# Kernel optimization log

Hardware: AMD Instinct MI355X
Metric: run time of the kernel (lower is better)

Reference implementation:

```python
import jax, jax.numpy as jnp
import numpy as np
from jax import lax

D = 256      # key/query dim
D_F = 256    # diff feature channels
C_TOK = 1    # leading context tokens in query_vit
EPS = 1e-6


def conv2d(x, w, b, pad):
    out = lax.conv_general_dilated(x, w, (1, 1), [(pad, pad), (pad, pad)],
                                   dimension_numbers=('NCHW', 'OIHW', 'NCHW'))
    return out + b[None, :, None, None]


def gn1(x, g, b):
    # GroupNorm with 1 group: normalize over (C,H,W) per sample
    mu = jnp.mean(x, axis=(1, 2, 3), keepdims=True)
    var = jnp.var(x, axis=(1, 2, 3), keepdims=True)
    xn = (x - mu) * lax.rsqrt(var + EPS)
    return xn * g[None, :, None, None] + b[None, :, None, None]


def resize_bilinear_ac(x, Ho, Wo):
    # F.interpolate(mode='bilinear', align_corners=True)
    B, C, H, W = x.shape
    ys = jnp.linspace(0.0, H - 1.0, Ho)
    xs = jnp.linspace(0.0, W - 1.0, Wo)
    y0 = jnp.floor(ys).astype(jnp.int32)
    y1 = jnp.minimum(y0 + 1, H - 1)
    wy = (ys - y0)[None, None, :, None]
    x0 = jnp.floor(xs).astype(jnp.int32)
    x1 = jnp.minimum(x0 + 1, W - 1)
    wx = (xs - x0)[None, None, None, :]
    r = x[:, :, y0, :] * (1.0 - wy) + x[:, :, y1, :] * wy
    return r[:, :, :, x0] * (1.0 - wx) + r[:, :, :, x1] * wx


def setup_inputs() -> dict:
    key = jax.random.key(0)
    ks = jax.random.split(key, 12)
    B, Hd, Wd, Ht, Wt = 8, 64, 64, 32, 32

    def kaiming(k, shape, fan_in):
        return jax.random.normal(k, shape, jnp.float32) * np.sqrt(2.0 / fan_in)

    return {
        'query_vit': jax.random.normal(ks[0], (B, C_TOK + Ht * Wt, D), jnp.float32),
        'feat_diff_cat': jax.random.normal(ks[1], (B, 5 * D_F, Hd, Wd), jnp.float32),
        'rb_w1': kaiming(ks[2], (D_F, 5 * D_F, 3, 3), 5 * D_F * 9), 'rb_b1': jnp.zeros((D_F,), jnp.float32),
        'rb_w2': kaiming(ks[3], (D_F, D_F, 3, 3), D_F * 9), 'rb_b2': jnp.zeros((D_F,), jnp.float32),
        'rb_ws': kaiming(ks[4], (D_F, 5 * D_F, 1, 1), 5 * D_F), 'rb_bs': jnp.zeros((D_F,), jnp.float32),
        'ln_g': jnp.ones((D_F,), jnp.float32), 'ln_b': jnp.zeros((D_F,), jnp.float32),
        'key_w': kaiming(ks[5], (D, D_F, 1, 1), D_F), 'key_b': jnp.zeros((D,), jnp.float32),
        'val_w': kaiming(ks[6], (D_F, D_F, 1, 1), D_F), 'val_b': jnp.zeros((D_F,), jnp.float32),
        'dh0_w': kaiming(ks[7], (D_F, D_F, 3, 3), D_F * 9), 'dh0_b': jnp.zeros((D_F,), jnp.float32),
        'dh1_w': kaiming(ks[8], (D_F, D_F, 3, 3), D_F * 9), 'dh1_b': jnp.zeros((D_F,), jnp.float32),
    }


def reference(query_vit, feat_diff_cat, rb_w1, rb_b1, rb_w2, rb_b2, rb_ws, rb_bs,
              ln_g, ln_b, key_w, key_b, val_w, val_b, dh0_w, dh0_b, dh1_w, dh1_b):
    B, _, h_diff, w_diff = feat_diff_cat.shape
    N = query_vit.shape[1] - C_TOK
    h_trm = w_trm = int(N ** 0.5)

    # ResBlock_ysh(D_f*5 -> D_f): conv3x3 + relu + conv3x3, 1x1-projected residual
    h = jax.nn.relu(conv2d(feat_diff_cat, rb_w1, rb_b1, 1))
    h = conv2d(h, rb_w2, rb_b2, 1)
    feat_diff = jax.nn.relu(h + conv2d(feat_diff_cat, rb_ws, rb_bs, 0))

    fln = gn1(feat_diff, ln_g, ln_b)
    key_diff = conv2d(fln, key_w, key_b, 0).reshape(B, D, -1)          # (B, D, HW)
    value_diff = conv2d(fln, val_w, val_b, 0).reshape(B, D_F, -1)      # (B, Df, HW)
    value_diff = jnp.transpose(value_diff, (0, 2, 1))                  # (B, HW, Df)

    # cross attention: (B, C+N, D) @ (B, D, HW) -> softmax -> @ (B, HW, Df)
    scores = jnp.einsum('bnd,bdm->bnm', query_vit, key_diff) * (D ** -0.5)
    attn = jax.nn.softmax(scores, axis=-1)
    out_cross = jnp.einsum('bnm,bmf->bnf', attn, value_diff)           # (B, C+N, Df)

    out_cross_c = out_cross[:, :C_TOK, :]
    out_p = jnp.transpose(out_cross[:, C_TOK:, :], (0, 2, 1)).reshape(B, D_F, h_trm, w_trm)
    out_p = jax.nn.relu(conv2d(out_p, dh0_w, dh0_b, 1))
    out_p = resize_bilinear_ac(out_p, h_diff, w_diff)
    out_p = out_p + feat_diff                                          # DropPath(0) = identity
    out_p = jax.nn.relu(conv2d(gn1(out_p, ln_g, ln_b), dh1_w, dh1_b, 1)) + out_p
    return out_cross_c, out_p
```

## Files before the change

### kernel.cpp

```cpp
#include <hip/hip_runtime.h>
#include <cstdint>
#include <cstddef>

typedef __attribute__((ext_vector_type(4))) float     f32x4;
typedef __attribute__((ext_vector_type(8))) __bf16    bf16x8;
typedef __attribute__((ext_vector_type(8))) short     short8;
typedef __attribute__((ext_vector_type(4))) unsigned short u16x4;
typedef unsigned short u16;

__device__ __forceinline__ float b2f(u16 u) {
  unsigned x = ((unsigned)u) << 16;
  float f;
  __builtin_memcpy(&f, &x, 4);
  return f;
}
__device__ __forceinline__ u16 f2b(float f) {
  unsigned u;
  __builtin_memcpy(&u, &f, 4);
  return (u16)((u + 0x7FFFu + ((u >> 16) & 1u)) >> 16);
}

struct GP {
  const u16*  A;
  const u16*  B;
  const float* bias;
  const void* aux;
  void*       C;
  float*      out0;
  float*      st;
  long long   aBS, bBS, cBS, auxBS, biasBS;
  int Ktot, Mrows, ldc;
  int cin, logW, wpad, poff;
  float scale;
};

#define GLDS16(g, l)                                                        \
  __builtin_amdgcn_global_load_lds(                                         \
      (const void __attribute__((address_space(1)))*)(g),                   \
      (void __attribute__((address_space(3)))*)(l), 16, 0, 0)

struct G256 {
  const u16* A;
  const u16* B;
  float* P;
  long long aBS;
  int Ktot, cin, logW, wpad, poff;
};

__global__ __launch_bounds__(512, 2) void k_gemm256(G256 gp) {
  const int tid = threadIdx.x;
  const int l = tid & 63, w = tid >> 6;
  const int lr = l & 15, lc = l >> 4;
  const int id = blockIdx.x;
  const int xcd = id & 7, slot = id >> 3;
  const int sp = xcd >> 2;
  const int u = (xcd & 3) * 32 + slot;
  const int mt = u & 15;
  const int b = u >> 4;
  const int m0 = mt << 8;
  const int wm = w >> 2, wn = w & 3;

  __shared__ __align__(16) u16 sm[2][32768];
  u16* smb = &sm[0][0];

  f32x4 acc[8][4];
#pragma unroll
  for (int i = 0; i < 8; ++i)
#pragma unroll
    for (int j = 0; j < 4; ++j) acc[i][j] = (f32x4){0.f, 0.f, 0.f, 0.f};

  const u16* Ab = gp.A + (size_t)b * gp.aBS;
  const int slotl = l & 3;
  const u16* aS[2];
  const u16* bS[2];
#pragma unroll
  for (int j = 0; j < 2; ++j) {
    const int r = j * 128 + w * 16 + (l >> 2);
    const int p = m0 + r;
    const int y = p >> gp.logW, x = p & ((1 << gp.logW) - 1);
    const int sw = (slotl ^ ((r >> 1) & 3)) << 3;
    aS[j] = Ab + (size_t)((y + gp.poff) * gp.wpad + (x + gp.poff)) * gp.cin + sw;
    bS[j] = gp.B + (size_t)r * gp.Ktot + sw;
  }
  auto dstA = [&](int buf, int ks, int j) -> u16* {
    return smb + buf * 32768 + ks * 8192 + (j * 128 + w * 16) * 32 + l * 8;
  };
  auto dstB = [&](int buf, int ks, int j) -> u16* {
    return smb + buf * 32768 + 16384 + ks * 8192 + (j * 128 + w * 16) * 32 + l * 8;
  };

  const int Thalf = (gp.Ktot >> 6) >> 1;
  const int kt0 = sp * Thalf;
  int off = kt0 << 6;
  int tap = off / gp.cin;
  int kcS = off - tap * gp.cin;
  int dxS = tap % 3;
  int tapS = (tap / 3) * gp.wpad + dxS;
  int ktS = kt0;

  auto adv = [&](int& kA, int& kB) {
    kB = ktS << 6;
    kA = tapS * gp.cin + kcS;
    kcS += 64;
    if (kcS == gp.cin) {
      kcS = 0; ++dxS; ++tapS;
      if (dxS == 3) { dxS = 0; tapS += gp.wpad - 3; }
    }
    ++ktS;
  };

  {
    int kA, kB;
    adv(kA, kB);
    GLDS16(aS[0] + kA, dstA(0, 0, 0));
    GLDS16(aS[1] + kA, dstA(0, 0, 1));
    GLDS16(bS[0] + kB, dstB(0, 0, 0));
    GLDS16(bS[1] + kB, dstB(0, 0, 1));
    GLDS16(aS[0] + kA + 32, dstA(0, 1, 0));
    GLDS16(aS[1] + kA + 32, dstA(0, 1, 1));
    GLDS16(bS[0] + kB + 32, dstB(0, 1, 0));
    GLDS16(bS[1] + kB + 32, dstB(0, 1, 1));
  }
  asm volatile("s_waitcnt vmcnt(0)" ::: "memory");
  __builtin_amdgcn_s_barrier();

  const int NT = Thalf;
  for (int t = 0; t < NT; ++t) {
    const int buf = t & 1;
    const char* base = (const char*)smb + buf * 65536;
    const bool pf = (t + 1 < NT);
    if (pf) {
      int kA, kB;
      adv(kA, kB);
      GLDS16(aS[0] + kA, dstA(buf ^ 1, 0, 0));
      GLDS16(aS[1] + kA, dstA(buf ^ 1, 0, 1));
      GLDS16(bS[0] + kB, dstB(buf ^ 1, 0, 0));
      GLDS16(bS[1] + kB, dstB(buf ^ 1, 0, 1));
      GLDS16(aS[0] + kA + 32, dstA(buf ^ 1, 1, 0));
      GLDS16(aS[1] + kA + 32, dstA(buf ^ 1, 1, 1));
      GLDS16(bS[0] + kB + 32, dstB(buf ^ 1, 1, 0));
      GLDS16(bS[1] + kB + 32, dstB(buf ^ 1, 1, 1));
    }
    bf16x8 bv0[4], bv1[4];
#pragma unroll
    for (int ni = 0; ni < 4; ++ni) {
      const int row = wn * 64 + ni * 16 + lr;
      const int sw = (lc ^ ((row >> 1) & 3)) << 4;
      bv0[ni] = *(const bf16x8*)(base + 32768 + row * 64 + sw);
      bv1[ni] = *(const bf16x8*)(base + 49152 + row * 64 + sw);
    }
#pragma unroll
    for (int mq = 0; mq < 2; ++mq) {
      bf16x8 a0[4], a1[4];
#pragma unroll
      for (int mi = 0; mi < 4; ++mi) {
        const int row = wm * 128 + (mq * 4 + mi) * 16 + lr;
        const int sw = (lc ^ ((row >> 1) & 3)) << 4;
        a0[mi] = *(const bf16x8*)(base + row * 64 + sw);
        a1[mi] = *(const bf16x8*)(base + 16384 + row * 64 + sw);
      }
#pragma unroll
      for (int mi = 0; mi < 4; ++mi)
#pragma unroll
        for (int ni = 0; ni < 4; ++ni)
          acc[mq * 4 + mi][ni] = __builtin_amdgcn_mfma_f32_16x16x32_bf16(
              a0[mi], bv0[ni], acc[mq * 4 + mi][ni], 0, 0, 0);
#pragma unroll
      for (int mi = 0; mi < 4; ++mi)
#pragma unroll
        for (int ni = 0; ni < 4; ++ni)
          acc[mq * 4 + mi][ni] = __builtin_amdgcn_mfma_f32_16x16x32_bf16(
              a1[mi], bv1[ni], acc[mq * 4 + mi][ni], 0, 0, 0);
    }
    asm volatile("s_waitcnt vmcnt(0)" ::: "memory");
    __builtin_amdgcn_s_barrier();
  }

  float* P = gp.P + ((size_t)sp * 128 + b * 16 + mt) * 65536;
#pragma unroll
  for (int mi = 0; mi < 8; ++mi)
#pragma unroll
    for (int ni = 0; ni < 4; ++ni) {
      const int ncol = wn * 64 + ni * 16 + lr;
      const int mloc = wm * 128 + mi * 16 + lc * 4;
#pragma unroll
      for (int r = 0; r < 4; ++r)
        P[(size_t)(mloc + r) * 256 + ncol] = acc[mi][ni][r];
    }
}

__global__ __launch_bounds__(256) void k_reduceH1(const float* __restrict__ P,
                                                  const float* __restrict__ bias,
                                                  u16* __restrict__ o) {
  const int i4 = blockIdx.x * 256 + threadIdx.x;
  const int flat = i4 << 2;
  const int n0 = flat & 255;
  const int mloc = (flat >> 8) & 255;
  const int gm = flat >> 16;
  const f32x4 a = *(const f32x4*)(P + (size_t)gm * 65536 + mloc * 256 + n0);
  const f32x4 c = *(const f32x4*)(P + (size_t)(128 + gm) * 65536 + mloc * 256 + n0);
  const f32x4 bb = *(const f32x4*)(bias + n0);
  const int batch = gm >> 4;
  const int mg = (gm & 15) * 256 + mloc;
  const int y = mg >> 6, x = mg & 63;
  u16x4 r;
#pragma unroll
  for (int k = 0; k < 4; ++k) r[k] = f2b(fmaxf(a[k] + c[k] + bb[k], 0.f));
  *(u16x4*)(o + ((size_t)batch * 4356 + (size_t)(y + 1) * 66 + x + 1) * 256 + n0) = r;
}

template <int AMODE, int CW>
__global__ __launch_bounds__(512, 2) void k_gemm8(GP gp) {
  const int tid = threadIdx.x;
  const int l = tid & 63, w = tid >> 6;
  const int b = blockIdx.z;
  const int m0 = blockIdx.x * 128;
  const int wm = w >> 2, wn = w & 3;
  const int lr = l & 15, lc = l >> 4;

  __shared__ __align__(16) u16 sm[2][24576];

  f32x4 acc[4][4];
#pragma unroll
  for (int i = 0; i < 4; ++i)
#pragma unroll
    for (int j = 0; j < 4; ++j) acc[i][j] = (f32x4){0.f, 0.f, 0.f, 0.f};

  const u16* Ab = gp.A + (size_t)b * gp.aBS;
  const u16* Bb = gp.B + (size_t)b * gp.bBS;
  const int scoff = (((tid & 7) ^ ((tid >> 3) & 7)) << 3);

  const u16* aP[2];
  const u16* aP2[2];
#pragma unroll
  for (int i = 0; i < 2; ++i) {
    const int p = m0 + i * 64 + (tid >> 3);
    const int y = p >> 6, x = p & 63;
    aP[i] = Ab + (size_t)(y * 66 + x) * gp.cin + scoff;
    if (AMODE == 2) {
      const u16* Xb = (const u16*)gp.aux + (size_t)b * gp.auxBS;
      aP2[i] = Xb + (size_t)((y + 1) * 66 + (x + 1)) * 1280 + scoff;
    }
  }
  const u16* bP[4];
#pragma unroll
  for (int i = 0; i < 4; ++i)
    bP[i] = Bb + (size_t)(i * 64 + (tid >> 3)) * gp.Ktot + scoff;

  const int NT = gp.Ktot >> 6;
  const int seg1t = (AMODE == 2) ? 36 : 0x7fffffff;
  int kcS = 0, tapS = 0, dxS = 0, nstg = 0;

  auto stage = [&](int buf) {
    const int kt = nstg++;
    const int kB = kt << 6;
    u16* sA = &sm[buf][0] + (w << 9);
    u16* sB = &sm[buf][8192] + (w << 9);
    if (AMODE == 2 && kt >= seg1t) {
      const int kA = (kt - seg1t) << 6;
      GLDS16(aP2[0] + kA, sA);
      GLDS16(aP2[1] + kA, sA + 4096);
    } else {
      const int kA = tapS * gp.cin + kcS;
      kcS += 64;
      if (kcS == gp.cin) {
        kcS = 0; ++dxS; ++tapS;
        if (dxS == 3) { dxS = 0; tapS += 63; }
      }
      GLDS16(aP[0] + kA, sA);
      GLDS16(aP[1] + kA, sA + 4096);
    }
    GLDS16(bP[0] + kB, sB);
    GLDS16(bP[1] + kB, sB + 4096);
    GLDS16(bP[2] + kB, sB + 8192);
    GLDS16(bP[3] + kB, sB + 12288);
  };

  stage(0);
  asm volatile("s_waitcnt vmcnt(0)" ::: "memory");
  __builtin_amdgcn_s_barrier();

  for (int t = 0; t < NT; ++t) {
    const int buf = t & 1;
    const u16* sAc = &sm[buf][0];
    const u16* sBc = &sm[buf][8192];
    if (t + 1 < NT) stage(buf ^ 1);

    bf16x8 av0[4], av1[4], bv0[4], bv1[4];
#pragma unroll
    for (int mi = 0; mi < 4; ++mi) {
      const int row = wm * 64 + mi * 16 + lr;
      av0[mi] = *(const bf16x8*)(sAc + row * 64 + (((0 + lc) ^ (row & 7)) << 3));
      av1[mi] = *(const bf16x8*)(sAc + row * 64 + (((4 + lc) ^ (row & 7)) << 3));
    }
#pragma unroll
    for (int ni = 0; ni < 4; ++ni) {
      const int row = wn * 64 + ni * 16 + lr;
      bv0[ni] = *(const bf16x8*)(sBc + row * 64 + (((0 + lc) ^ (row & 7)) << 3));
      bv1[ni] = *(const bf16x8*)(sBc + row * 64 + (((4 + lc) ^ (row & 7)) << 3));
    }
#pragma unroll
    for (int mi = 0; mi < 4; ++mi)
#pragma unroll
      for (int ni = 0; ni < 4; ++ni)
        acc[mi][ni] = __builtin_amdgcn_mfma_f32_16x16x32_bf16(
            av0[mi], bv0[ni], acc[mi][ni], 0, 0, 0);
#pragma unroll
    for (int mi = 0; mi < 4; ++mi)
#pragma unroll
      for (int ni = 0; ni < 4; ++ni)
        acc[mi][ni] = __builtin_amdgcn_mfma_f32_16x16x32_bf16(
            av1[mi], bv1[ni], acc[mi][ni], 0, 0, 0);
    asm volatile("s_waitcnt vmcnt(0)" ::: "memory");
    __builtin_amdgcn_s_barrier();
  }

  float lsum = 0.f, lsq = 0.f;
#pragma unroll
  for (int mi = 0; mi < 4; ++mi) {
#pragma unroll
    for (int ni = 0; ni < 4; ++ni) {
      const int ncol = wn * 64 + ni * 16 + lr;
      const int mbase = m0 + wm * 64 + mi * 16 + lc * 4;
      const float bv_ = gp.bias[ncol];
      if constexpr (CW == 8) {
        float* F = (float*)gp.C + (size_t)b * gp.cBS;
        u16* FB = (u16*)gp.out0 + (size_t)b * gp.cBS;
#pragma unroll
        for (int r = 0; r < 4; ++r) {
          float v = fmaxf(acc[mi][ni][r] + bv_, 0.f);
          const size_t idx = (size_t)(mbase + r) * 256 + ncol;
          F[idx] = v;
          FB[idx] = f2b(v);
          lsum += v;
          lsq += v * v;
        }
      } else {
        float* Cf =
            (float*)gp.C + (size_t)b * gp.cBS + (size_t)ncol * 4096 + mbase;
        const float* mid = (const float*)gp.aux + (size_t)b * gp.auxBS;
        f32x4 o;
#pragma unroll
        for (int r = 0; r < 4; ++r) {
          float v = fmaxf(acc[mi][ni][r] + bv_, 0.f);
          o[r] = v + mid[(size_t)(mbase + r) * 256 + ncol];
        }
        *(f32x4*)Cf = o;
      }
    }
  }
  if constexpr (CW == 8) {
    __syncthreads();
#pragma unroll
    for (int o = 32; o; o >>= 1) {
      lsum += __shfl_down(lsum, o);
      lsq += __shfl_down(lsq, o);
    }
    float* red = (float*)&sm[0][0];
    if (l == 0) { red[w * 2] = lsum; red[w * 2 + 1] = lsq; }
    __syncthreads();
    if (tid == 0) {
      float s = 0.f, s2 = 0.f;
#pragma unroll
      for (int k = 0; k < 8; ++k) { s += red[k * 2]; s2 += red[k * 2 + 1]; }
      atomicAdd(&gp.st[b * 2], s);
      atomicAdd(&gp.st[b * 2 + 1], s2);
    }
  }
}

template <int AMODE, int CW, bool RELU>
__global__ __launch_bounds__(256, 2) void k_gemm(GP gp) {
  const int tid = threadIdx.x;
  const int l = tid & 63, w = tid >> 6;
  const int b = blockIdx.z;
  const int m0 = blockIdx.x * 128, n0 = blockIdx.y * 128;
  const int wm = w >> 1, wn = w & 1;

  __shared__ __align__(16) u16 smA[128 * 64];
  __shared__ __align__(16) u16 smB[128 * 64];

  f32x4 acc[4][4];
#pragma unroll
  for (int i = 0; i < 4; ++i)
#pragma unroll
    for (int j = 0; j < 4; ++j) acc[i][j] = (f32x4){0.f, 0.f, 0.f, 0.f};

  const u16* Ab = gp.A + (size_t)b * gp.aBS;
  const u16* Bb = gp.B + (size_t)b * gp.bBS;

  const int scoff = (((l & 7) ^ (l >> 3)) << 3);

  const u16* aRow[4];
  const u16* bRow[4];
  u16* ldsA[4];
  u16* ldsB[4];
#pragma unroll
  for (int i = 0; i < 4; ++i) {
    const int r = w * 32 + i * 8 + (l >> 3);
    bRow[i] = Bb + (size_t)(n0 + r) * gp.Ktot + scoff;
    const int p = m0 + r;
    if (AMODE == 0) {
      const int pc = p < gp.Mrows ? p : gp.Mrows - 1;
      aRow[i] = Ab + (size_t)pc * gp.Ktot + scoff;
    } else {
      const int y = p >> gp.logW, x = p & ((1 << gp.logW) - 1);
      const int icoord = (y + gp.poff) * gp.wpad + (x + gp.poff);
      aRow[i] = Ab + (size_t)icoord * gp.cin + scoff;
    }
    ldsA[i] = smA + (w * 32 + i * 8) * 64;
    ldsB[i] = smB + (w * 32 + i * 8) * 64;
  }

  const int ktiles = gp.Ktot >> 6;
  int tap_off = 0, dx = 0, kc = 0;

  for (int kt = 0; kt < ktiles; ++kt) {
    int koffA;
    if (AMODE == 0)
      koffA = kt << 6;
    else
      koffA = tap_off * gp.cin + kc;
    const int koffB = kt << 6;
#pragma unroll
    for (int i = 0; i < 4; ++i) GLDS16(aRow[i] + koffA, ldsA[i]);
#pragma unroll
    for (int i = 0; i < 4; ++i) GLDS16(bRow[i] + koffB, ldsB[i]);

    if (AMODE == 1) {
      kc += 64;
      if (kc == gp.cin) {
        kc = 0;
        ++dx;
        ++tap_off;
        if (dx == 3) { dx = 0; tap_off += gp.wpad - 3; }
      }
    }

    __syncthreads();
#pragma unroll
    for (int ks = 0; ks < 2; ++ks) {
      bf16x8 av[4], bv[4];
      const int cc = (ks << 2) + (l >> 4);
#pragma unroll
      for (int mi = 0; mi < 4; ++mi) {
        const int row = wm * 64 + mi * 16 + (l & 15);
        av[mi] = *(const bf16x8*)((const char*)smA + (row << 7) +
                                  ((cc ^ (row & 7)) << 4));
      }
#pragma unroll
      for (int ni = 0; ni < 4; ++ni) {
        const int row = wn * 64 + ni * 16 + (l & 15);
        bv[ni] = *(const bf16x8*)((const char*)smB + (row << 7) +
                                  ((cc ^ (row & 7)) << 4));
      }
#pragma unroll
      for (int mi = 0; mi < 4; ++mi)
#pragma unroll
        for (int ni = 0; ni < 4; ++ni)
          acc[mi][ni] = __builtin_amdgcn_mfma_f32_16x16x32_bf16(
              av[mi], bv[ni], acc[mi][ni], 0, 0, 0);
    }
    __syncthreads();
  }

#pragma unroll
  for (int mi = 0; mi < 4; ++mi) {
#pragma unroll
    for (int ni = 0; ni < 4; ++ni) {
      const int ncol = n0 + wn * 64 + ni * 16 + (l & 15);
      const int mbase = m0 + wm * 64 + mi * 16 + ((l >> 4) << 2);
      const float bv_ =
          gp.bias ? gp.bias[(size_t)b * gp.biasBS + ncol] : 0.f;

      if constexpr (CW == 7) {
        u16* base = (u16*)gp.C;
        if (ncol < 256) {
#pragma unroll
          for (int r = 0; r < 4; ++r)
            base[(size_t)b * 1048576 + (size_t)(mbase + r) * 256 + ncol] =
                f2b(acc[mi][ni][r] + bv_);
        } else {
          u16x4 pk;
#pragma unroll
          for (int r = 0; r < 4; ++r) pk[r] = f2b(acc[mi][ni][r] + bv_);
          *(u16x4*)(base + 8388608 + (size_t)b * 1048576 +
                    (size_t)(ncol - 256) * 4096 + mbase) = pk;
        }
      } else {
#pragma unroll
        for (int reg = 0; reg < 4; ++reg) {
          const int mrow = mbase + reg;
          if (mrow >= gp.Mrows) continue;
          float v = acc[mi][ni][reg] * gp.scale + bv_;
          if (RELU) v = v > 0.f ? v : 0.f;
          if constexpr (CW == 0) {
            ((u16*)gp.C)[(size_t)b * gp.cBS + (size_t)mrow * gp.ldc + ncol] =
                f2b(v);
          } else if constexpr (CW == 4) {
            if (mrow == 0) {
              gp.out0[(size_t)b * 256 + ncol] = v;
            } else {
              const int p = mrow - 1, y = p >> 5, x = p & 31;
              ((u16*)gp.C)[(size_t)b * gp.cBS +
                           (size_t)((y + 1) * 34 + (x + 1)) * 256 + ncol] =
                  f2b(v);
            }
          } else if constexpr (CW == 5) {
            ((float*)gp.C)[(size_t)b * gp.cBS + (size_t)mrow * 256 + ncol] = v;
          }
        }
      }
    }
  }
}


__global__ __launch_bounds__(256) void k_prep_x(const float* __restrict__ x,
                                                u16* __restrict__ o) {
  __shared__ float t[32][65];
  const int b = blockIdx.z, c0 = blockIdx.y << 5, y = blockIdx.x;
  const float* src = x + ((size_t)b * 1280 + c0) * 4096 + (size_t)y * 64;
#pragma unroll
  for (int i = 0; i < 8; ++i) {
    const int idx = threadIdx.x + (i << 8);
    const int c = idx >> 6, xx = idx & 63;
    t[c][xx] = src[(size_t)c * 4096 + xx];
  }
  __syncthreads();
  u16* dst = o + ((size_t)b * 4356 + (size_t)(y + 1) * 66 + 1) * 1280 + c0;
  const int xx = threadIdx.x >> 2;
  const int cq = (threadIdx.x & 3) << 3;
  short8 pk;
#pragma unroll
  for (int j = 0; j < 8; ++j) pk[j] = (short)f2b(t[cq + j][xx]);
  *(short8*)(dst + (size_t)xx * 1280 + cq) = pk;
}

__device__ __forceinline__ void zb1(u16* p, int P, int C, int idx) {
  const int per_img = (4 * P - 4) * C;
  const int b = idx / per_img;
  const int r = idx % per_img;
  const int pix = r / C, c = r % C;
  int y, x;
  const int Pm = P - 1;
  if (pix < P) { y = 0; x = pix; }
  else if (pix < 2 * P) { y = Pm; x = pix - P; }
  else if (pix < 3 * P - 2) { y = pix - 2 * P + 1; x = 0; }
  else { y = pix - (3 * P - 2) + 1; x = Pm; }
  p[((size_t)b * P * P + (size_t)y * P + x) * C + c] = 0;
}

__global__ __launch_bounds__(256) void k_zero_borders(u16* XPAD, u16* H1,
                                                      u16* G2, u16* OCP) {
  const int nx = 8 * 260 * 1280;
  const int nh = 8 * 260 * 256;
  const int no = 8 * 132 * 256;
  const int total = nx + 2 * nh + no;
  for (int i = blockIdx.x * 256 + threadIdx.x; i < total;
       i += gridDim.x * 256) {
    if (i < nx) zb1(XPAD, 66, 1280, i);
    else if (i < nx + nh) zb1(H1, 66, 256, i - nx);
    else if (i < nx + 2 * nh) zb1(G2, 66, 256, i - nx - nh);
    else zb1(OCP, 34, 256, i - nx - 2 * nh);
  }
}

__global__ __launch_bounds__(256) void k_prep_all(
    const float* __restrict__ w1, const float* __restrict__ w2,
    const float* __restrict__ wsc, const float* __restrict__ wd0,
    const float* __restrict__ wd1, const float* __restrict__ b2,
    const float* __restrict__ bsc, const float* __restrict__ q,
    u16* __restrict__ W1R, u16* __restrict__ WCAT2, u16* __restrict__ WD0R,
    u16* __restrict__ WD1R, float* __restrict__ BB2, u16* __restrict__ QB) {
  const int N1 = 2949120, N2 = 917504, N3 = 589824, N4 = 589824,
            N5 = 2099200, N6 = 256;
  const int T = N1 + N2 + N3 + N4 + N5 + N6;
  for (int i = blockIdx.x * 256 + threadIdx.x; i < T; i += gridDim.x * 256) {
    if (i < N1) {
      const int ci = i % 1280, r = i / 1280, t = r % 9, co = r / 9;
      W1R[i] = f2b(w1[((size_t)co * 1280 + ci) * 9 + t]);
    } else if (i < N1 + N2) {
      const int k = i - N1;
      const int co = k / 3584, kk = k % 3584;
      float v;
      if (kk < 2304) {
        const int tap = kk / 256, ci = kk % 256;
        v = w2[((size_t)co * 256 + ci) * 9 + tap];
      } else {
        v = wsc[(size_t)co * 1280 + (kk - 2304)];
      }
      WCAT2[k] = f2b(v);
    } else if (i < N1 + N2 + N3) {
      const int k = i - N1 - N2;
      const int ci = k % 256, r = k / 256, t = r % 9, co = r / 9;
      WD0R[k] = f2b(wd0[((size_t)co * 256 + ci) * 9 + t]);
    } else if (i < N1 + N2 + N3 + N4) {
      const int k = i - N1 - N2 - N3;
      const int ci = k % 256, r = k / 256, t = r % 9, co = r / 9;
      WD1R[k] = f2b(wd1[((size_t)co * 256 + ci) * 9 + t]);
    } else if (i < N1 + N2 + N3 + N4 + N5) {
      const int k = i - N1 - N2 - N3 - N4;
      QB[k] = f2b(q[k] * 0.0625f);
    } else {
      const int k = i - N1 - N2 - N3 - N4 - N5;
      BB2[k] = b2[k] + bsc[k];
    }
  }
}

__global__ __launch_bounds__(256) void k_foldkv(
    const float* __restrict__ wk, const float* __restrict__ wv,
    const float* __restrict__ bk, const float* __restrict__ bv,
    const float* __restrict__ g, const float* __restrict__ lnb,
    const float* __restrict__ st, u16* __restrict__ WKVB,
    float* __restrict__ BKVB) {
  const int idx = blockIdx.x * 256 + threadIdx.x;
  const int b = idx >> 9, j = idx & 511;
  const float mu = st[b * 2] * (1.f / 1048576.f);
  const float var = st[b * 2 + 1] * (1.f / 1048576.f) - mu * mu;
  const float rs = rsqrtf(var + 1e-6f);
  const float* wrow = (j < 256) ? wk + (size_t)j * 256 : wv + (size_t)(j - 256) * 256;
  float acc = (j < 256) ? bk[j] : bv[j - 256];
  u16* orow = WKVB + ((size_t)b * 512 + j) * 256;
  for (int c = 0; c < 256; ++c) {
    const float wv_ = wrow[c];
    orow[c] = f2b(wv_ * g[c] * rs);
    acc += wv_ * (lnb[c] - mu * rs * g[c]);
  }
  BKVB[b * 512 + j] = acc;
}

template <bool PAD>
__global__ __launch_bounds__(256) void k_gn_norm(const float* __restrict__ x,
                                                 const float* __restrict__ st,
                                                 const float* __restrict__ g,
                                                 const float* __restrict__ bb,
                                                 u16* __restrict__ o) {
  const int b = blockIdx.y;
  const float mu = st[b * 2] * (1.f / 1048576.f);
  const float var = st[b * 2 + 1] * (1.f / 1048576.f) - mu * mu;
  const float rs = rsqrtf(var + 1e-6f);
  const int i4 = blockIdx.x * 256 + threadIdx.x;
  const f32x4 v = ((const f32x4*)(x + (size_t)b * 1048576))[i4];
  const int flat = i4 << 2;
  const int c = flat & 255;
  const int p = flat >> 8;
  const f32x4 gv = *(const f32x4*)(g + c);
  const f32x4 bv = *(const f32x4*)(bb + c);
  u16x4 r;
#pragma unroll
  for (int k = 0; k < 4; ++k) r[k] = f2b((v[k] - mu) * rs * gv[k] + bv[k]);
  size_t oidx;
  if (PAD) {
    const int y = p >> 6, xx = p & 63;
    oidx = ((size_t)b * 4356 + (size_t)(y + 1) * 66 + xx + 1) * 256 + c;
  } else {
    oidx = ((size_t)b * 4096 + p) * 256 + c;
  }
  *(u16x4*)(o + oidx) = r;
}

__global__ __launch_bounds__(256) void k_softmax(u16* __restrict__ s) {
  const size_t row = blockIdx.x;
  u16* p = s + row * 4096;
  const int t = threadIdx.x;
  const short8 r0 = ((const short8*)p)[t];
  const short8 r1 = ((const short8*)p)[t + 256];
  float v[16];
#pragma unroll
  for (int i = 0; i < 8; ++i) {
    v[i] = b2f((u16)r0[i]);
    v[8 + i] = b2f((u16)r1[i]);
  }
  float m = v[0];
#pragma unroll
  for (int i = 1; i < 16; ++i) m = fmaxf(m, v[i]);
#pragma unroll
  for (int o = 32; o; o >>= 1) m = fmaxf(m, __shfl_xor(m, o));
  __shared__ float lm[4], lsum[4];
  const int w = t >> 6;
  if ((t & 63) == 0) lm[w] = m;
  __syncthreads();
  m = fmaxf(fmaxf(lm[0], lm[1]), fmaxf(lm[2], lm[3]));
  float sum = 0.f;
#pragma unroll
  for (int i = 0; i < 16; ++i) {
    v[i] = __expf(v[i] - m);
    sum += v[i];
  }
#pragma unroll
  for (int o = 32; o; o >>= 1) sum += __shfl_xor(sum, o);
  if ((t & 63) == 0) lsum[w] = sum;
  __syncthreads();
  sum = lsum[0] + lsum[1] + lsum[2] + lsum[3];
  const float inv = 1.f / sum;
  short8 o0, o1;
#pragma unroll
  for (int i = 0; i < 8; ++i) {
    o0[i] = (short)f2b(v[i] * inv);
    o1[i] = (short)f2b(v[8 + i] * inv);
  }
  ((short8*)p)[t] = o0;
  ((short8*)p)[t + 256] = o1;
}

__global__ __launch_bounds__(256) void k_resize_add(const float* __restrict__ d0,
                                                    const float* __restrict__ F,
                                                    float* __restrict__ mid,
                                                    float* __restrict__ st) {
  const int b = blockIdx.y;
  const float* db = d0 + (size_t)b * 262144;
  const float* Fb = F + (size_t)b * 1048576;
  float* mb = mid + (size_t)b * 1048576;
  float ls = 0.f, lq = 0.f;
  for (int i4 = blockIdx.x * 256 + threadIdx.x; i4 < 262144;
       i4 += 64 * 256) {
    const int flat = i4 << 2;
    const int c = flat & 255;
    const int p = flat >> 8;
    const int y = p >> 6, x = p & 63;
    const float fy = y * (31.f / 63.f);
    const int y0 = (int)fy;
    const float wy = fy - y0;
    const int y1 = y0 + 1 > 31 ? 31 : y0 + 1;
    const float fx = x * (31.f / 63.f);
    const int x0 = (int)fx;
    const float wx = fx - x0;
    const int x1 = x0 + 1 > 31 ? 31 : x0 + 1;
    const f32x4 a = *(const f32x4*)(db + ((size_t)(y0 * 32 + x0) << 8) + c);
    const f32x4 bq = *(const f32x4*)(db + ((size_t)(y0 * 32 + x1) << 8) + c);
    const f32x4 cq = *(const f32x4*)(db + ((size_t)(y1 * 32 + x0) << 8) + c);
    const f32x4 dq = *(const f32x4*)(db + ((size_t)(y1 * 32 + x1) << 8) + c);
    f32x4 r = (a * (1.f - wx) + bq * wx) * (1.f - wy) +
              (cq * (1.f - wx) + dq * wx) * wy;
    r += *(const f32x4*)(Fb + flat);
    *(f32x4*)(mb + flat) = r;
    ls += r[0] + r[1] + r[2] + r[3];
    lq += r[0] * r[0] + r[1] * r[1] + r[2] * r[2] + r[3] * r[3];
  }
#pragma unroll
  for (int o = 32; o; o >>= 1) {
    ls += __shfl_down(ls, o);
    lq += __shfl_down(lq, o);
  }
  __shared__ float red[8];
  const int w = threadIdx.x >> 6;
  if ((threadIdx.x & 63) == 0) { red[w * 2] = ls; red[w * 2 + 1] = lq; }
  __syncthreads();
  if (threadIdx.x == 0) {
    atomicAdd(&st[16 + b * 2], red[0] + red[2] + red[4] + red[6]);
    atomicAdd(&st[16 + b * 2 + 1], red[1] + red[3] + red[5] + red[7]);
  }
}


extern "C" void kernel_launch(void* const* d_in, const int* in_sizes, int n_in,
                              void* d_out, int out_size, void* d_ws,
                              size_t ws_size, hipStream_t stream) {
  (void)in_sizes; (void)n_in; (void)out_size;

  const float* q   = (const float*)d_in[0];
  const float* xdc = (const float*)d_in[1];
  const float* w1  = (const float*)d_in[2];
  const float* b1  = (const float*)d_in[3];
  const float* w2  = (const float*)d_in[4];
  const float* b2  = (const float*)d_in[5];
  const float* wsc = (const float*)d_in[6];
  const float* bsc = (const float*)d_in[7];
  const float* lng = (const float*)d_in[8];
  const float* lnb = (const float*)d_in[9];
  const float* wk  = (const float*)d_in[10];
  const float* bk  = (const float*)d_in[11];
  const float* wv  = (const float*)d_in[12];
  const float* bv  = (const float*)d_in[13];
  const float* wd0 = (const float*)d_in[14];
  const float* bd0 = (const float*)d_in[15];
  const float* wd1 = (const float*)d_in[16];
  const float* bd1 = (const float*)d_in[17];

  char* ws = (char*)d_ws;
  size_t cur = 0;
  auto alloc = [&](size_t sz) {
    char* p = ws + cur;
    cur += sz;
    return p;
  };
  u16* XPAD  = (u16*)alloc(89194496);
  u16* W1R   = (u16*)alloc(5898240);
  u16* WCAT2 = (u16*)alloc(1835008);
  u16* WD0R  = (u16*)alloc(1179648);
  u16* WD1R  = (u16*)alloc(1179648);
  u16* WKVB  = (u16*)alloc(2097152);
  float* BKVB = (float*)alloc(16384);
  float* BB2 = (float*)alloc(1024);
  u16* H1    = (u16*)alloc(17842176);
  float* F   = (float*)alloc(33554432);
  u16* FB    = (u16*)alloc(16777216);
  u16* KT    = (u16*)alloc(16777216);
  u16* V     = (u16*)alloc(16777216);
  u16* QB    = (u16*)alloc(4198400);
  u16* OCP   = (u16*)alloc(4734976);
  float* D0O = (float*)alloc(8388608);
  float* MID = (float*)alloc(33554432);
  u16* G2    = (u16*)alloc(17842176);
  float* ST  = (float*)alloc(256);
  u16* SCORES = XPAD;
  float* PART = (float*)F;
  (void)V;

  if (ws_size < cur) return;

  float* out0 = (float*)d_out;
  float* out1 = (float*)d_out + 2048;

  hipMemsetAsync(ST, 0, 256, stream);
  k_zero_borders<<<2048, 256, 0, stream>>>(XPAD, H1, G2, OCP);
  k_prep_x<<<dim3(64, 40, 8), 256, 0, stream>>>(xdc, XPAD);
  k_prep_all<<<4096, 256, 0, stream>>>(w1, w2, wsc, wd0, wd1, b2, bsc, q, W1R,
                                       WCAT2, WD0R, WD1R, BB2, QB);

  {
    G256 g{};
    g.A = XPAD; g.B = W1R; g.P = PART;
    g.aBS = 5575680; g.Ktot = 11520;
    g.cin = 1280; g.logW = 6; g.wpad = 66; g.poff = 0;
    k_gemm256<<<256, 512, 0, stream>>>(g);
    k_reduceH1<<<8192, 256, 0, stream>>>(PART, b1, H1);
  }
  {
    GP g{};
    g.A = H1; g.B = WCAT2; g.bias = BB2; g.aux = XPAD; g.C = F;
    g.out0 = (float*)FB; g.st = ST;
    g.aBS = 1115136; g.bBS = 0; g.cBS = 1048576; g.auxBS = 5575680;
    g.Ktot = 3584; g.Mrows = 4096; g.ldc = 256;
    g.cin = 256; g.logW = 6; g.wpad = 66; g.poff = 0; g.scale = 1.f;
    k_gemm8<2, 8><<<dim3(32, 1, 8), 512, 0, stream>>>(g);
  }
  k_foldkv<<<16, 256, 0, stream>>>(wk, wv, bk, bv, lng, lnb, ST, WKVB, BKVB);
  {
    GP g{};
    g.A = FB; g.B = WKVB; g.bias = BKVB; g.C = KT;
    g.aBS = 1048576; g.bBS = 131072; g.cBS = 0; g.biasBS = 512;
    g.Ktot = 256; g.Mrows = 4096; g.ldc = 256; g.scale = 1.f;
    k_gemm<0, 7, false><<<dim3(32, 4, 8), 256, 0, stream>>>(g);
  }
  {
    GP g{};
    g.A = QB; g.B = KT; g.bias = nullptr; g.C = SCORES;
    g.aBS = 262400; g.bBS = 1048576; g.cBS = 4198400;
    g.Ktot = 256; g.Mrows = 1025; g.ldc = 4096; g.scale = 1.f;
    k_gemm<0, 0, false><<<dim3(9, 32, 8), 256, 0, stream>>>(g);
  }
  k_softmax<<<8200, 256, 0, stream>>>(SCORES);
  {
    GP g{};
    g.A = SCORES; g.B = V; g.bias = nullptr; g.C = OCP; g.out0 = out0;
    g.aBS = 4198400; g.bBS = 1048576; g.cBS = 295936;
    g.Ktot = 4096; g.Mrows = 1025; g.ldc = 256; g.scale = 1.f;
    k_gemm<0, 4, false><<<dim3(9, 2, 8), 256, 0, stream>>>(g);
  }
  {
    GP g{};
    g.A = OCP; g.B = WD0R; g.bias = bd0; g.C = D0O;
    g.aBS = 295936; g.bBS = 0; g.cBS = 262144; g.biasBS = 0;
    g.Ktot = 2304; g.Mrows = 1024; g.ldc = 256;
    g.cin = 256; g.logW = 5; g.wpad = 34; g.poff = 0; g.scale = 1.f;
    k_gemm<1, 5, true><<<dim3(8, 2, 8), 256, 0, stream>>>(g);
  }
  k_resize_add<<<dim3(64, 8), 256, 0, stream>>>(D0O, F, MID, ST);
  k_gn_norm<true><<<dim3(1024, 8), 256, 0, stream>>>(MID, ST + 16, lng, lnb, G2);
  {
    GP g{};
    g.A = G2; g.B = WD1R; g.bias = bd1; g.C = out1; g.aux = MID;
    g.aBS = 1115136; g.bBS = 0; g.cBS = 1048576; g.auxBS = 1048576;
    g.Ktot = 2304; g.Mrows = 4096; g.ldc = 256;
    g.cin = 256; g.logW = 6; g.wpad = 66; g.poff = 0; g.scale = 1.f;
    k_gemm8<1, 6><<<dim3(32, 1, 8), 512, 0, stream>>>(g);
  }
}
```

Measured before the change: 700.0 us.

## Use 4-slot ring of K=32 stages with three loads in flight in conv GEMM

```diff
diff --git a/kernel.cpp b/kernel.cpp
--- a/kernel.cpp
+++ b/kernel.cpp
@@ -60,7 +60,7 @@
   const int m0 = mt << 8;
   const int wm = w >> 2, wn = w & 3;
 
-  __shared__ __align__(16) u16 sm[2][32768];
+  __shared__ __align__(16) u16 sm[4][16384];
   u16* smb = &sm[0][0];
 
   f32x4 acc[8][4];
@@ -70,7 +70,6 @@
     for (int j = 0; j < 4; ++j) acc[i][j] = (f32x4){0.f, 0.f, 0.f, 0.f};
 
   const u16* Ab = gp.A + (size_t)b * gp.aBS;
-  const int slotl = l & 3;
   const u16* aS[2];
   const u16* bS[2];
 #pragma unroll
@@ -78,102 +77,80 @@
     const int r = j * 128 + w * 16 + (l >> 2);
     const int p = m0 + r;
     const int y = p >> gp.logW, x = p & ((1 << gp.logW) - 1);
-    const int sw = (slotl ^ ((r >> 1) & 3)) << 3;
+    const int sw = ((l & 3) ^ ((r >> 1) & 3)) << 3;
     aS[j] = Ab + (size_t)((y + gp.poff) * gp.wpad + (x + gp.poff)) * gp.cin + sw;
     bS[j] = gp.B + (size_t)r * gp.Ktot + sw;
   }
-  auto dstA = [&](int buf, int ks, int j) -> u16* {
-    return smb + buf * 32768 + ks * 8192 + (j * 128 + w * 16) * 32 + l * 8;
-  };
-  auto dstB = [&](int buf, int ks, int j) -> u16* {
-    return smb + buf * 32768 + 16384 + ks * 8192 + (j * 128 + w * 16) * 32 + l * 8;
-  };
-
-  const int Thalf = (gp.Ktot >> 6) >> 1;
-  const int kt0 = sp * Thalf;
-  int off = kt0 << 6;
+
+  const int NH = gp.Ktot >> 6;
+  const int kt0h = sp * NH;
+  {
+  }
+  int off = kt0h << 5;
   int tap = off / gp.cin;
   int kcS = off - tap * gp.cin;
   int dxS = tap % 3;
   int tapS = (tap / 3) * gp.wpad + dxS;
-  int ktS = kt0;
-
-  auto adv = [&](int& kA, int& kB) {
-    kB = ktS << 6;
-    kA = tapS * gp.cin + kcS;
-    kcS += 64;
+  int hgS = kt0h;
+
+  auto stage = [&](int h) {
+    const int hb = h & 3;
+    const int kB = hgS << 5;
+    const int kA = tapS * gp.cin + kcS;
+    kcS += 32;
     if (kcS == gp.cin) {
       kcS = 0; ++dxS; ++tapS;
       if (dxS == 3) { dxS = 0; tapS += gp.wpad - 3; }
     }
-    ++ktS;
+    ++hgS;
+    u16* base = smb + hb * 16384 + (w * 16) * 32 + l * 8;
+    GLDS16(aS[0] + kA, base);
+    GLDS16(aS[1] + kA, base + 4096);
+    GLDS16(bS[0] + kB, base + 8192);
+    GLDS16(bS[1] + kB, base + 12288);
   };
 
-  {
-    int kA, kB;
-    adv(kA, kB);
-    GLDS16(aS[0] + kA, dstA(0, 0, 0));
-    GLDS16(aS[1] + kA, dstA(0, 0, 1));
-    GLDS16(bS[0] + kB, dstB(0, 0, 0));
-    GLDS16(bS[1] + kB, dstB(0, 0, 1));
-    GLDS16(aS[0] + kA + 32, dstA(0, 1, 0));
-    GLDS16(aS[1] + kA + 32, dstA(0, 1, 1));
-    GLDS16(bS[0] + kB + 32, dstB(0, 1, 0));
-    GLDS16(bS[1] + kB + 32, dstB(0, 1, 1));
-  }
-  asm volatile("s_waitcnt vmcnt(0)" ::: "memory");
+  stage(0);
+  stage(1);
+  stage(2);
+  asm volatile("s_waitcnt vmcnt(8)" ::: "memory");
   __builtin_amdgcn_s_barrier();
 
-  const int NT = Thalf;
-  for (int t = 0; t < NT; ++t) {
-    const int buf = t & 1;
-    const char* base = (const char*)smb + buf * 65536;
-    const bool pf = (t + 1 < NT);
-    if (pf) {
-      int kA, kB;
-      adv(kA, kB);
-      GLDS16(aS[0] + kA, dstA(buf ^ 1, 0, 0));
-      GLDS16(aS[1] + kA, dstA(buf ^ 1, 0, 1));
-      GLDS16(bS[0] + kB, dstB(buf ^ 1, 0, 0));
-      GLDS16(bS[1] + kB, dstB(buf ^ 1, 0, 1));
-      GLDS16(aS[0] + kA + 32, dstA(buf ^ 1, 1, 0));
-      GLDS16(aS[1] + kA + 32, dstA(buf ^ 1, 1, 1));
-      GLDS16(bS[0] + kB + 32, dstB(buf ^ 1, 1, 0));
-      GLDS16(bS[1] + kB + 32, dstB(buf ^ 1, 1, 1));
-    }
-    bf16x8 bv0[4], bv1[4];
+  for (int h = 0; h < NH; ++h) {
+    const int hb = h & 3;
+    if (h + 3 < NH) stage(h + 3);
+
+    const char* base = (const char*)smb + hb * 32768;
+    bf16x8 av[8], bv[4];
+#pragma unroll
+    for (int mi = 0; mi < 8; ++mi) {
+      const int row = wm * 128 + mi * 16 + lr;
+      const int sw = (lc ^ ((row >> 1) & 3)) << 4;
+      av[mi] = *(const bf16x8*)(base + row * 64 + sw);
+    }
 #pragma unroll
     for (int ni = 0; ni < 4; ++ni) {
       const int row = wn * 64 + ni * 16 + lr;
       const int sw = (lc ^ ((row >> 1) & 3)) << 4;
-      bv0[ni] = *(const bf16x8*)(base + 32768 + row * 64 + sw);
-      bv1[ni] = *(const bf16x8*)(base + 49152 + row * 64 + sw);
-    }
-#pragma unroll
-    for (int mq = 0; mq < 2; ++mq) {
-      bf16x8 a0[4], a1[4];
-#pragma unroll
-      for (int mi = 0; mi < 4; ++mi) {
-        const int row = wm * 128 + (mq * 4 + mi) * 16 + lr;
-        const int sw = (lc ^ ((row >> 1) & 3)) << 4;
-        a0[mi] = *(const bf16x8*)(base + row * 64 + sw);
-        a1[mi] = *(const bf16x8*)(base + 16384 + row * 64 + sw);
-      }
-#pragma unroll
-      for (int mi = 0; mi < 4; ++mi)
-#pragma unroll
-        for (int ni = 0; ni < 4; ++ni)
-          acc[mq * 4 + mi][ni] = __builtin_amdgcn_mfma_f32_16x16x32_bf16(
-              a0[mi], bv0[ni], acc[mq * 4 + mi][ni], 0, 0, 0);
-#pragma unroll
-      for (int mi = 0; mi < 4; ++mi)
-#pragma unroll
-        for (int ni = 0; ni < 4; ++ni)
-          acc[mq * 4 + mi][ni] = __builtin_amdgcn_mfma_f32_16x16x32_bf16(
-              a1[mi], bv1[ni], acc[mq * 4 + mi][ni], 0, 0, 0);
-    }
-    asm volatile("s_waitcnt vmcnt(0)" ::: "memory");
-    __builtin_amdgcn_s_barrier();
+      bv[ni] = *(const bf16x8*)(base + 16384 + row * 64 + sw);
+    }
+#pragma unroll
+    for (int mi = 0; mi < 8; ++mi)
+#pragma unroll
+      for (int ni = 0; ni < 4; ++ni)
+        acc[mi][ni] = __builtin_amdgcn_mfma_f32_16x16x32_bf16(
+            av[mi], bv[ni], acc[mi][ni], 0, 0, 0);
+
+    const int rem = NH - 1 - h;
+    if (rem > 0) {
+      if (rem > 2)
+        asm volatile("s_waitcnt vmcnt(8)" ::: "memory");
+      else if (rem == 2)
+        asm volatile("s_waitcnt vmcnt(4)" ::: "memory");
+      else
+        asm volatile("s_waitcnt vmcnt(0)" ::: "memory");
+      __builtin_amdgcn_s_barrier();
+    }
   }
 
   float* P = gp.P + ((size_t)sp * 128 + b * 16 + mt) * 65536;
```

Result: no change. 697.3 us (-0.4%).
